# Kernel tuning notes

Measured on AMD Instinct MI355X. Metric: run time of the kernel, lower is better.

## Reference

```python
import jax, jax.numpy as jnp
import numpy as np

EPS = 1e-5
NUM_HEADS = 12


def setup_inputs() -> dict:
    key = jax.random.key(0)
    ks = jax.random.split(key, 4)
    B, S, E = 8, 1024, 768
    x = jax.random.normal(ks[0], (B, S, E), dtype=jnp.float32)
    ln_w = jnp.ones((E,), dtype=jnp.float32)
    ln_b = jnp.zeros((E,), dtype=jnp.float32)
    # PyTorch packed in-projection [3E, E]; scale ~ Xavier-ish
    in_proj_w = jax.random.normal(ks[1], (3 * E, E), dtype=jnp.float32) * (1.0 / np.sqrt(E))
    in_proj_b = jnp.zeros((3 * E,), dtype=jnp.float32)
    out_proj_w = jax.random.normal(ks[2], (E, E), dtype=jnp.float32) * (1.0 / np.sqrt(E))
    out_proj_b = jnp.zeros((E,), dtype=jnp.float32)
    return {"x": x, "ln_w": ln_w, "ln_b": ln_b,
            "in_proj_w": in_proj_w, "in_proj_b": in_proj_b,
            "out_proj_w": out_proj_w, "out_proj_b": out_proj_b}


def reference(x, ln_w, ln_b, in_proj_w, in_proj_b, out_proj_w, out_proj_b):
    B, S, E = x.shape
    H = NUM_HEADS
    D = E // H
    # LayerNorm over last dim (eps matches torch default 1e-5)
    mu = jnp.mean(x, axis=-1, keepdims=True)
    var = jnp.mean((x - mu) ** 2, axis=-1, keepdims=True)
    xn = (x - mu) * jax.lax.rsqrt(var + EPS) * ln_w + ln_b
    # Packed QKV projection: [B,S,3E]
    qkv = jnp.einsum('bse,fe->bsf', xn, in_proj_w) + in_proj_b
    q, k, v = jnp.split(qkv, 3, axis=-1)
    # [B,H,S,D]
    q = q.reshape(B, S, H, D).transpose(0, 2, 1, 3)
    k = k.reshape(B, S, H, D).transpose(0, 2, 1, 3)
    v = v.reshape(B, S, H, D).transpose(0, 2, 1, 3)
    scale = 1.0 / jnp.sqrt(jnp.asarray(D, dtype=x.dtype))
    # Explicit scores [B,H,S,S] — matches the non-flash need_weights path
    scores = jnp.einsum('bhqd,bhkd->bhqk', q * scale, k)
    attn = jax.nn.softmax(scores, axis=-1)
    ctx = jnp.einsum('bhqk,bhkd->bhqd', attn, v)  # [B,H,S,D]
    ctx = ctx.transpose(0, 2, 1, 3).reshape(B, S, E)
    out = jnp.einsum('bse,fe->bsf', ctx, out_proj_w) + out_proj_b
    return out
```

## Files before the change

### kernel.cpp

```cpp
#include <hip/hip_runtime.h>
#include <cstdint>

typedef _Float16 half8 __attribute__((ext_vector_type(8)));
typedef _Float16 half4v __attribute__((ext_vector_type(4)));
typedef float f32x4 __attribute__((ext_vector_type(4)));

#define AS1(p) (const __attribute__((address_space(1))) void*)(p)
#define AS3(p) (__attribute__((address_space(3))) void*)(p)

__device__ __forceinline__ void gl_lds16(const _Float16* g, _Float16* l) {
  __builtin_amdgcn_global_load_lds(AS1(g), AS3(l), 16, 0, 0);
}

__device__ __forceinline__ f32x4 mfma16(half8 a, half8 b, f32x4 c) {
  return __builtin_amdgcn_mfma_f32_16x16x32_f16(a, b, c, 0, 0, 0);
}

__global__ void conv_f32_f16(const float* __restrict__ s, _Float16* __restrict__ d, int n4) {
  int i = blockIdx.x * 256 + threadIdx.x;
  int stride = gridDim.x * 256;
  for (; i < n4; i += stride) {
    float4 v = ((const float4*)s)[i];
    half4v o = { (_Float16)v.x, (_Float16)v.y, (_Float16)v.z, (_Float16)v.w };
    *(half4v*)(d + (size_t)i * 4) = o;
  }
}

__global__ __launch_bounds__(256) void ln_kernel(const float* __restrict__ x,
    const float* __restrict__ g, const float* __restrict__ be, _Float16* __restrict__ xn) {
  const int row = blockIdx.x, tid = threadIdx.x;
  const float* xr = x + (size_t)row * 768;
  float v0 = xr[tid], v1 = xr[tid + 256], v2 = xr[tid + 512];
  float s = v0 + v1 + v2;
  float ss = v0 * v0 + v1 * v1 + v2 * v2;
  __shared__ float red[8];
  const int w = tid >> 6, l = tid & 63;
  #pragma unroll
  for (int o = 32; o > 0; o >>= 1) { s += __shfl_down(s, o); ss += __shfl_down(ss, o); }
  if (l == 0) { red[w] = s; red[4 + w] = ss; }
  __syncthreads();
  s  = red[0] + red[1] + red[2] + red[3];
  ss = red[4] + red[5] + red[6] + red[7];
  float mu = s * (1.0f / 768.0f);
  float var = ss * (1.0f / 768.0f) - mu * mu;
  float rs = rsqrtf(var + 1e-5f);
  _Float16* xo = xn + (size_t)row * 768;
  xo[tid]       = (_Float16)((v0 - mu) * rs * g[tid]       + be[tid]);
  xo[tid + 256] = (_Float16)((v1 - mu) * rs * g[tid + 256] + be[tid + 256]);
  xo[tid + 512] = (_Float16)((v2 - mu) * rs * g[tid + 512] + be[tid + 512]);
}

template<int EPI>
__global__ __launch_bounds__(256) void gemm_bt(
    const _Float16* __restrict__ A, const _Float16* __restrict__ Bw,
    const float* __restrict__ bias,
    _Float16* __restrict__ qh, _Float16* __restrict__ kh, _Float16* __restrict__ vh,
    float* __restrict__ outp, int M, int N, int K) {
  __shared__ _Float16 As[128 * 32];
  __shared__ _Float16 Bs[128 * 32];
  const int tid = threadIdx.x;
  const int w = tid >> 6, l = tid & 63;
  const int wr = w >> 1, wc = w & 1;
  const int l15 = l & 15, lg = l >> 4;
  const int bn = blockIdx.x, bm = blockIdx.y;
  const _Float16* Ab = A + (size_t)bm * 128 * K;
  const _Float16* Bb = Bw + (size_t)bn * 128 * K;
  f32x4 acc[4][4];
  #pragma unroll
  for (int m = 0; m < 4; ++m)
    #pragma unroll
    for (int n = 0; n < 4; ++n) acc[m][n] = (f32x4){0.f, 0.f, 0.f, 0.f};

  for (int kt = 0; kt < K; kt += 32) {
    #pragma unroll
    for (int j = 0; j < 2; ++j) {
      const int c = j * 256 + tid;
      const int r = c >> 2, kc = (c & 3) * 8;
      gl_lds16(Ab + (size_t)r * K + kt + kc, &As[(j * 256 + w * 64) * 8]);
      gl_lds16(Bb + (size_t)r * K + kt + kc, &Bs[(j * 256 + w * 64) * 8]);
    }
    __syncthreads();
    half8 af[4], bf[4];
    #pragma unroll
    for (int m = 0; m < 4; ++m) af[m] = *(const half8*)&As[(wr * 64 + m * 16 + l15) * 32 + lg * 8];
    #pragma unroll
    for (int n = 0; n < 4; ++n) bf[n] = *(const half8*)&Bs[(wc * 64 + n * 16 + l15) * 32 + lg * 8];
    #pragma unroll
    for (int m = 0; m < 4; ++m)
      #pragma unroll
      for (int n = 0; n < 4; ++n) acc[m][n] = mfma16(af[m], bf[n], acc[m][n]);
    __syncthreads();
  }

  const int rowb = bm * 128 + wr * 64;
  const int colb = bn * 128 + wc * 64;
  if (EPI == 0) {
    const int t = (bn * 128) / 768;
    _Float16* dst = (t == 0) ? qh : (t == 1) ? kh : vh;
    const float qscale = (t == 0) ? 0.125f * 1.44269504088896f : 1.0f;
    #pragma unroll
    for (int m = 0; m < 4; ++m)
      #pragma unroll
      for (int n = 0; n < 4; ++n)
        #pragma unroll
        for (int r = 0; r < 4; ++r) {
          const int gr = rowb + m * 16 + lg * 4 + r;
          const int f  = colb + n * 16 + l15;
          const float val = (acc[m][n][r] + bias[f]) * qscale;
          const int fb = f - t * 768;
          const int hh = fb >> 6, dd = fb & 63;
          const int b_ = gr >> 10, s_ = gr & 1023;
          dst[(((size_t)b_ * 12 + hh) * 1024 + s_) * 64 + dd] = (_Float16)val;
        }
  } else {
    #pragma unroll
    for (int m = 0; m < 4; ++m)
      #pragma unroll
      for (int n = 0; n < 4; ++n)
        #pragma unroll
        for (int r = 0; r < 4; ++r) {
          const int gr = rowb + m * 16 + lg * 4 + r;
          const int f  = colb + n * 16 + l15;
          outp[(size_t)gr * 768 + f] = acc[m][n][r] + bias[f];
        }
  }
}

__global__ __launch_bounds__(256) void transpose_v(const _Float16* __restrict__ v,
                                                   _Float16* __restrict__ vt) {
  __shared__ _Float16 t[64][72];
  const int scb = blockIdx.x, bh = blockIdx.y;
  const int tid = threadIdx.x;
  const _Float16* vp = v + (size_t)bh * 1024 * 64 + (size_t)scb * 64 * 64;
  #pragma unroll
  for (int j = 0; j < 2; ++j) {
    const int c = j * 256 + tid;
    const int r = c >> 3, d = (c & 7) * 8;
    *(half8*)&t[r][d] = *(const half8*)&vp[(size_t)r * 64 + d];
  }
  __syncthreads();
  #pragma unroll
  for (int j = 0; j < 2; ++j) {
    const int c = j * 256 + tid;
    const int d = c >> 3, s0 = (c & 7) * 8;
    half8 o;
    #pragma unroll
    for (int x = 0; x < 8; ++x) o[x] = t[s0 + x][d];
    *(half8*)&vt[((size_t)bh * 64 + d) * 1024 + scb * 64 + s0] = o;
  }
}

__global__ __launch_bounds__(256) void attn_fused(
    const _Float16* __restrict__ qg, const _Float16* __restrict__ kg,
    const _Float16* __restrict__ vtg, _Float16* __restrict__ ctx) {
  __shared__ _Float16 Kt[64 * 72];
  __shared__ _Float16 Vt[64 * 72];
  __shared__ _Float16 Pt[128 * 72];
  const int bh = blockIdx.x, qt = blockIdx.y;
  const int b_ = bh / 12, h = bh % 12;
  const _Float16* qp = qg + (size_t)bh * 1024 * 64 + (size_t)qt * 128 * 64;
  const _Float16* kp = kg + (size_t)bh * 1024 * 64;
  const _Float16* vp = vtg + (size_t)bh * 64 * 1024;
  const int tid = threadIdx.x, w = tid >> 6, l = tid & 63;
  const int l15 = l & 15, lg = l >> 4;
  const int cs = (tid >> 3);
  const int cd = (tid & 7) * 8;

  #pragma unroll
  for (int j = 0; j < 4; ++j) {
    const int c = j * 256 + tid;
    const int r = c >> 3, dc = (c & 7) * 8;
    *(half8*)&Pt[r * 72 + dc] = *(const half8*)&qp[(size_t)r * 64 + dc];
  }
  __syncthreads();
  half8 qa[2][2];
  #pragma unroll
  for (int m = 0; m < 2; ++m)
    #pragma unroll
    for (int kk = 0; kk < 2; ++kk)
      qa[m][kk] = *(const half8*)&Pt[(w * 32 + m * 16 + l15) * 72 + kk * 32 + lg * 8];

  f32x4 acc[2][4];
  float Lx[2];
  #pragma unroll
  for (int m = 0; m < 2; ++m) {
    #pragma unroll
    for (int n = 0; n < 4; ++n) acc[m][n] = (f32x4){0.f, 0.f, 0.f, 0.f};
    Lx[m] = 0.f;
  }

  half8 kr[2], vr[2];
  #pragma unroll
  for (int j = 0; j < 2; ++j) {
    kr[j] = *(const half8*)&kp[(size_t)(cs + j * 32) * 64 + cd];
    vr[j] = *(const half8*)&vp[(size_t)(cs + j * 32) * 1024 + cd];
  }

  for (int kt = 0; kt < 16; ++kt) {
    __syncthreads();
    #pragma unroll
    for (int j = 0; j < 2; ++j) {
      *(half8*)&Kt[(cs + j * 32) * 72 + cd] = kr[j];
      *(half8*)&Vt[(cs + j * 32) * 72 + cd] = vr[j];
    }
    if (kt < 15) {
      #pragma unroll
      for (int j = 0; j < 2; ++j) {
        kr[j] = *(const half8*)&kp[((size_t)(kt + 1) * 64 + cs + j * 32) * 64 + cd];
        vr[j] = *(const half8*)&vp[(size_t)(cs + j * 32) * 1024 + (kt + 1) * 64 + cd];
      }
    }
    __syncthreads();

    f32x4 sc[2][4];
    #pragma unroll
    for (int m = 0; m < 2; ++m)
      #pragma unroll
      for (int n = 0; n < 4; ++n) sc[m][n] = (f32x4){0.f, 0.f, 0.f, 0.f};
    #pragma unroll
    for (int n = 0; n < 4; ++n)
      #pragma unroll
      for (int kk = 0; kk < 2; ++kk) {
        const half8 kb = *(const half8*)&Kt[(n * 16 + l15) * 72 + kk * 32 + lg * 8];
        #pragma unroll
        for (int m = 0; m < 2; ++m) sc[m][n] = mfma16(kb, qa[m][kk], sc[m][n]);
      }

    #pragma unroll
    for (int m = 0; m < 2; ++m) {
      #pragma unroll
      for (int n = 0; n < 4; ++n) {
        half4v ph;
        #pragma unroll
        for (int r = 0; r < 4; ++r) {
          const float p = exp2f(sc[m][n][r]);
          Lx[m] += p;
          ph[r] = (_Float16)p;
        }
        *(half4v*)&Pt[(w * 32 + m * 16 + l15) * 72 + n * 16 + lg * 4] = ph;
      }
    }

    #pragma unroll
    for (int kk = 0; kk < 2; ++kk) {
      half8 pa[2];
      #pragma unroll
      for (int m = 0; m < 2; ++m)
        pa[m] = *(const half8*)&Pt[(w * 32 + m * 16 + l15) * 72 + kk * 32 + lg * 8];
      #pragma unroll
      for (int nd = 0; nd < 4; ++nd) {
        const half8 vb = *(const half8*)&Vt[(nd * 16 + l15) * 72 + kk * 32 + lg * 8];
        #pragma unroll
        for (int m = 0; m < 2; ++m) acc[m][nd] = mfma16(pa[m], vb, acc[m][nd]);
      }
    }
  }

  #pragma unroll
  for (int m = 0; m < 2; ++m) {
    Lx[m] += __shfl_xor(Lx[m], 16);
    Lx[m] += __shfl_xor(Lx[m], 32);
  }
  float rv[2][4];
  #pragma unroll
  for (int m = 0; m < 2; ++m)
    #pragma unroll
    for (int r = 0; r < 4; ++r) rv[m][r] = 1.0f / __shfl(Lx[m], lg * 4 + r);
  #pragma unroll
  for (int m = 0; m < 2; ++m)
    #pragma unroll
    for (int nd = 0; nd < 4; ++nd)
      #pragma unroll
      for (int r = 0; r < 4; ++r) {
        const int rl = w * 32 + m * 16 + lg * 4 + r;
        const int s_ = qt * 128 + rl;
        const int dd = nd * 16 + l15;
        const float o = acc[m][nd][r] * rv[m][r];
        ctx[((size_t)b_ * 1024 + s_) * 768 + h * 64 + dd] = (_Float16)o;
      }
}

extern "C" void kernel_launch(void* const* d_in, const int* in_sizes, int n_in,
                              void* d_out, int out_size, void* d_ws, size_t ws_size,
                              hipStream_t stream) {
  const float* x     = (const float*)d_in[0];
  const float* ln_w  = (const float*)d_in[1];
  const float* ln_b  = (const float*)d_in[2];
  const float* w_in  = (const float*)d_in[3];
  const float* b_in  = (const float*)d_in[4];
  const float* w_out = (const float*)d_in[5];
  const float* b_out = (const float*)d_in[6];
  float* out = (float*)d_out;

  _Float16* ws = (_Float16*)d_ws;
  const size_t SZ = (size_t)8192 * 768;
  _Float16* xn   = ws;
  _Float16* wi16 = xn + SZ;
  _Float16* wo16 = wi16 + (size_t)2304 * 768;
  _Float16* qh   = wo16 + (size_t)768 * 768;
  _Float16* kh   = qh + SZ;
  _Float16* vh   = kh + SZ;
  _Float16* vth  = vh + SZ;
  _Float16* ctxh = vth + SZ;

  conv_f32_f16<<<1024, 256, 0, stream>>>(w_in, wi16, (2304 * 768) / 4);
  conv_f32_f16<<<576, 256, 0, stream>>>(w_out, wo16, (768 * 768) / 4);
  ln_kernel<<<8192, 256, 0, stream>>>(x, ln_w, ln_b, xn);
  gemm_bt<0><<<dim3(18, 64), 256, 0, stream>>>(xn, wi16, b_in, qh, kh, vh, nullptr, 8192, 2304, 768);
  transpose_v<<<dim3(16, 96), 256, 0, stream>>>(vh, vth);
  attn_fused<<<dim3(96, 8), 256, 0, stream>>>(qh, kh, vth, ctxh);
  gemm_bt<1><<<dim3(6, 64), 256, 0, stream>>>(ctxh, wo16, b_out, nullptr, nullptr, nullptr, out, 8192, 768, 768);
}
```

Before: 244.6 us.

## Double-buffer GEMM LDS tiles and remap blocks for XCD-local L2 reuse

```diff
diff --git a/kernel.cpp b/kernel.cpp
--- a/kernel.cpp
+++ b/kernel.cpp
@@ -56,13 +56,17 @@
     const float* __restrict__ bias,
     _Float16* __restrict__ qh, _Float16* __restrict__ kh, _Float16* __restrict__ vh,
     float* __restrict__ outp, int M, int N, int K) {
-  __shared__ _Float16 As[128 * 32];
-  __shared__ _Float16 Bs[128 * 32];
+  __shared__ _Float16 As[2][128 * 32];
+  __shared__ _Float16 Bs[2][128 * 32];
   const int tid = threadIdx.x;
   const int w = tid >> 6, l = tid & 63;
   const int wr = w >> 1, wc = w & 1;
   const int l15 = l & 15, lg = l >> 4;
-  const int bn = blockIdx.x, bm = blockIdx.y;
+  const int wg = blockIdx.x;
+  const int xcd = wg & 7;
+  const int idx = wg >> 3;
+  const int bn = idx >> 3;
+  const int bm = xcd * 8 + (idx & 7);
   const _Float16* Ab = A + (size_t)bm * 128 * K;
   const _Float16* Bb = Bw + (size_t)bn * 128 * K;
   f32x4 acc[4][4];
@@ -71,20 +75,32 @@
     #pragma unroll
     for (int n = 0; n < 4; ++n) acc[m][n] = (f32x4){0.f, 0.f, 0.f, 0.f};
 
-  for (int kt = 0; kt < K; kt += 32) {
-    #pragma unroll
-    for (int j = 0; j < 2; ++j) {
-      const int c = j * 256 + tid;
-      const int r = c >> 2, kc = (c & 3) * 8;
-      gl_lds16(Ab + (size_t)r * K + kt + kc, &As[(j * 256 + w * 64) * 8]);
-      gl_lds16(Bb + (size_t)r * K + kt + kc, &Bs[(j * 256 + w * 64) * 8]);
-    }
-    __syncthreads();
+  const int cA = tid >> 2, kcA = (tid & 3) * 8;
+
+  #pragma unroll
+  for (int j = 0; j < 2; ++j) {
+    const int r = j * 64 + cA;
+    gl_lds16(Ab + (size_t)r * K + kcA, &As[0][(j * 256 + w * 64) * 8]);
+    gl_lds16(Bb + (size_t)r * K + kcA, &Bs[0][(j * 256 + w * 64) * 8]);
+  }
+  __syncthreads();
+
+  const int nt = K >> 5;
+  for (int kt = 0; kt < nt; ++kt) {
+    const int cur = kt & 1;
+    if (kt + 1 < nt) {
+      #pragma unroll
+      for (int j = 0; j < 2; ++j) {
+        const int r = j * 64 + cA;
+        gl_lds16(Ab + (size_t)r * K + (kt + 1) * 32 + kcA, &As[cur ^ 1][(j * 256 + w * 64) * 8]);
+        gl_lds16(Bb + (size_t)r * K + (kt + 1) * 32 + kcA, &Bs[cur ^ 1][(j * 256 + w * 64) * 8]);
+      }
+    }
     half8 af[4], bf[4];
     #pragma unroll
-    for (int m = 0; m < 4; ++m) af[m] = *(const half8*)&As[(wr * 64 + m * 16 + l15) * 32 + lg * 8];
-    #pragma unroll
-    for (int n = 0; n < 4; ++n) bf[n] = *(const half8*)&Bs[(wc * 64 + n * 16 + l15) * 32 + lg * 8];
+    for (int m = 0; m < 4; ++m) af[m] = *(const half8*)&As[cur][(wr * 64 + m * 16 + l15) * 32 + lg * 8];
+    #pragma unroll
+    for (int n = 0; n < 4; ++n) bf[n] = *(const half8*)&Bs[cur][(wc * 64 + n * 16 + l15) * 32 + lg * 8];
     #pragma unroll
     for (int m = 0; m < 4; ++m)
       #pragma unroll
@@ -95,7 +111,7 @@
   const int rowb = bm * 128 + wr * 64;
   const int colb = bn * 128 + wc * 64;
   if (EPI == 0) {
-    const int t = (bn * 128) / 768;
+    const int t = bn / 6;
     _Float16* dst = (t == 0) ? qh : (t == 1) ? kh : vh;
     const float qscale = (t == 0) ? 0.125f * 1.44269504088896f : 1.0f;
     #pragma unroll
@@ -306,8 +322,8 @@
   conv_f32_f16<<<1024, 256, 0, stream>>>(w_in, wi16, (2304 * 768) / 4);
   conv_f32_f16<<<576, 256, 0, stream>>>(w_out, wo16, (768 * 768) / 4);
   ln_kernel<<<8192, 256, 0, stream>>>(x, ln_w, ln_b, xn);
-  gemm_bt<0><<<dim3(18, 64), 256, 0, stream>>>(xn, wi16, b_in, qh, kh, vh, nullptr, 8192, 2304, 768);
+  gemm_bt<0><<<1152, 256, 0, stream>>>(xn, wi16, b_in, qh, kh, vh, nullptr, 8192, 2304, 768);
   transpose_v<<<dim3(16, 96), 256, 0, stream>>>(vh, vth);
   attn_fused<<<dim3(96, 8), 256, 0, stream>>>(qh, kh, vth, ctxh);
-  gemm_bt<1><<<dim3(6, 64), 256, 0, stream>>>(ctxh, wo16, b_out, nullptr, nullptr, nullptr, out, 8192, 768, 768);
-}
+  gemm_bt<1><<<384, 256, 0, stream>>>(ctxh, wo16, b_out, nullptr, nullptr, nullptr, out, 8192, 768, 768);
+}
```

Result: faster. 230.7 us (-5.7%).
